# Performance work log

Hardware: AMD Instinct MI355X
Metric: run time of the kernel (lower is better)

## Reference

```python
import jax, jax.numpy as jnp
import numpy as np

GRID_SIZE = 5
SPLINE_ORDER = 3
# Extended knot grid over [-1, 1]: grid_size + 2*spline_order + 1 = 12 knots
_H = 2.0 / GRID_SIZE
GRID = (jnp.arange(-SPLINE_ORDER, GRID_SIZE + SPLINE_ORDER + 1, dtype=jnp.float32) * _H - 1.0)


def b_splines(x):
    # x: [N, F] -> bases [N, F, GRID_SIZE + SPLINE_ORDER]
    g = GRID.astype(x.dtype)
    xe = x[..., None]
    bases = ((xe >= g[:-1]) & (xe < g[1:])).astype(x.dtype)
    for k in range(1, SPLINE_ORDER + 1):
        left = (xe - g[: -(k + 1)]) / (g[k:-1] - g[: -(k + 1)]) * bases[..., :-1]
        right = (g[k + 1:] - xe) / (g[k + 1:] - g[1:-k]) * bases[..., 1:]
        bases = left + right
    return bases


def kan_conv(x, base_w, spline_w, spline_scaler):
    # x: [B, Cin, H, W]; 3x3 conv, stride 1, pad 1 -> [B, Cout, H, W]
    B, C, H, W = x.shape
    patches = jax.lax.conv_general_dilated_patches(
        x, (3, 3), (1, 1), [(1, 1), (1, 1)])  # [B, C*9, H, W]
    feat = patches.transpose(0, 2, 3, 1).reshape(B * H * W, C * 9)
    base_out = jax.nn.silu(feat) @ base_w.T  # [N, Cout]
    bas = b_splines(feat)                    # [N, C*9, 8]
    sw = spline_w * spline_scaler[..., None] # standalone spline scale
    spline_out = jnp.einsum('nik,oik->no', bas, sw)
    out = (base_out + spline_out).reshape(B, H, W, -1).transpose(0, 3, 1, 2)
    return out


def upsample2x(x):
    return jnp.repeat(jnp.repeat(x, 2, axis=2), 2, axis=3)


def setup_inputs() -> dict:
    key = jax.random.key(0)
    ks = jax.random.split(key, 16)
    d = {}
    d['x'] = jax.random.normal(ks[0], (64, 100), dtype=jnp.float32)
    d['lin_w'] = jax.random.normal(ks[1], (2048, 100), dtype=jnp.float32) * 0.1
    d['lin_b'] = jax.random.normal(ks[2], (2048,), dtype=jnp.float32) * 0.01
    chans = [(512, 256), (256, 128), (128, 64), (64, 3)]
    i = 3
    for li, (cin, cout) in enumerate(chans, start=1):
        fin = cin * 9
        scale = 1.0 / np.sqrt(fin)
        d[f'bw{li}'] = jax.random.normal(ks[i], (cout, fin), dtype=jnp.float32) * scale; i += 1
        d[f'sw{li}'] = jax.random.normal(ks[i], (cout, fin, GRID_SIZE + SPLINE_ORDER), dtype=jnp.float32) * (0.1 * scale); i += 1
        d[f'ss{li}'] = jax.random.normal(ks[i], (cout, fin), dtype=jnp.float32) * scale + 1.0; i += 1
    return d


def reference(x, lin_w, lin_b, bw1, sw1, ss1, bw2, sw2, ss2, bw3, sw3, ss3, bw4, sw4, ss4):
    h = jax.nn.relu(x @ lin_w.T + lin_b)          # [B, 2048]
    h = h.reshape(-1, 512, 2, 2)                  # Unflatten
    h = upsample2x(h)                             # 4x4
    h = kan_conv(h, bw1, sw1, ss1)                # [B,256,4,4]
    h = upsample2x(h)                             # 8x8
    h = kan_conv(h, bw2, sw2, ss2)                # [B,128,8,8]
    h = upsample2x(h)                             # 16x16
    h = kan_conv(h, bw3, sw3, ss3)                # [B,64,16,16]
    h = upsample2x(h)                             # 32x32
    h = kan_conv(h, bw4, sw4, ss4)                # [B,3,32,32]
    return jnp.tanh(h)
```

## Files before the change

### kernel.cpp

```cpp
#include <hip/hip_runtime.h>
#include <cstdint>
#include <cmath>

#define BATCH 64

typedef __attribute__((ext_vector_type(8))) __bf16 bf16x8;
typedef __attribute__((ext_vector_type(16))) float f32x16;

__device__ __forceinline__ void expand9(float x, float* e) {
  float t = __expf(-x);
  e[0] = __fdividef(x, 1.f + t);
  float b[11];
#pragma unroll
  for (int j = 0; j < 11; ++j) {
    float gj  = 0.4f * (float)j - 2.2f;
    float gj1 = 0.4f * (float)(j + 1) - 2.2f;
    b[j] = (x >= gj && x < gj1) ? 1.f : 0.f;
  }
#pragma unroll
  for (int k = 1; k <= 3; ++k) {
    float inv = 1.f / (0.4f * (float)k);
#pragma unroll
    for (int j = 0; j < 11 - k; ++j) {
      float gj   = 0.4f * (float)j - 2.2f;
      float gjk1 = 0.4f * (float)(j + k + 1) - 2.2f;
      b[j] = ((x - gj) * b[j] + (gjk1 - x) * b[j + 1]) * inv;
    }
  }
#pragma unroll
  for (int v = 0; v < 8; ++v) e[v + 1] = b[v];
}

__device__ __forceinline__ unsigned short f2bf(float x) {
  uint32_t u = __float_as_uint(x);
  uint32_t r = u + 0x7fffu + ((u >> 16) & 1u);
  return (unsigned short)(r >> 16);
}

__device__ __forceinline__ void pack9(const float* e, uint32_t* d) {
  d[0] = (uint32_t)f2bf(e[0]) | ((uint32_t)f2bf(e[1]) << 16);
  d[1] = (uint32_t)f2bf(e[2]) | ((uint32_t)f2bf(e[3]) << 16);
  d[2] = (uint32_t)f2bf(e[4]) | ((uint32_t)f2bf(e[5]) << 16);
  d[3] = (uint32_t)f2bf(e[6]) | ((uint32_t)f2bf(e[7]) << 16);
  d[4] = (uint32_t)f2bf(e[8]);
}

template <int F, int N, int LOGN>
__device__ __forceinline__ void bpack_body(int bid, const float* __restrict__ bw,
                                           const float* __restrict__ sw,
                                           const float* __restrict__ ss,
                                           unsigned short* __restrict__ Bg) {
  int idx = bid * 256 + threadIdx.x;
  int fl = idx & 15;
  int n = (idx >> 4) & (N - 1);
  int kc = idx >> (4 + LOGN);
  int f = kc * 16 + fl;
  size_t src = (size_t)n * F + f;
  float bv = bw[src];
  float sc = ss[src];
  const float4* sp = reinterpret_cast<const float4*>(sw + src * 8);
  float4 s0 = sp[0], s1 = sp[1];
  size_t base = ((size_t)(kc * 9) * N + n) * 16 + fl;
  const size_t vs = (size_t)N * 16;
  Bg[base]          = f2bf(bv);
  Bg[base + vs]     = f2bf(s0.x * sc);
  Bg[base + 2 * vs] = f2bf(s0.y * sc);
  Bg[base + 3 * vs] = f2bf(s0.z * sc);
  Bg[base + 4 * vs] = f2bf(s0.w * sc);
  Bg[base + 5 * vs] = f2bf(s1.x * sc);
  Bg[base + 6 * vs] = f2bf(s1.y * sc);
  Bg[base + 7 * vs] = f2bf(s1.z * sc);
  Bg[base + 8 * vs] = f2bf(s1.w * sc);
}

__device__ __forceinline__ void wnl4_body(int bid, const float* __restrict__ bw,
                                          const float* __restrict__ sw,
                                          const float* __restrict__ ss,
                                          float* __restrict__ Wn) {
  int idx = bid * 256 + threadIdx.x;
  if (idx >= 27648) return;
  int u = idx % 27;
  int o = u % 3, v = u / 3;
  int rest = idx / 27;
  int nb = rest & 3;
  rest >>= 2;
  int pc = rest & 3;
  rest >>= 2;
  int c = rest;
  int PH = pc >> 1, PW = pc & 1;
  int a = nb >> 1, b2 = nb & 1;
  float s = 0.f;
#pragma unroll
  for (int kh = 0; kh < 3; ++kh) {
    if (((kh > PH) ? 1 : 0) != a) continue;
#pragma unroll
    for (int kw = 0; kw < 3; ++kw) {
      if (((kw > PW) ? 1 : 0) != b2) continue;
      int f = c * 9 + kh * 3 + kw;
      float wv = (v == 0)
                     ? bw[o * 576 + f]
                     : sw[((size_t)(o * 576 + f)) * 8 + (v - 1)] * ss[o * 576 + f];
      s += wv;
    }
  }
  Wn[idx] = s;
}

__device__ __forceinline__ void linear_body(int bid, const float* __restrict__ x,
                                            const float* __restrict__ w,
                                            const float* __restrict__ bias,
                                            float* __restrict__ h,
                                            uint32_t* __restrict__ E) {
  int idx = bid * 256 + threadIdx.x;
  int b = idx >> 11, o = idx & 2047;
  const float* xr = x + b * 100;
  const float* wr = w + o * 100;
  float acc = bias[o];
#pragma unroll 4
  for (int k = 0; k < 100; ++k) acc += xr[k] * wr[k];
  float hv = fmaxf(acc, 0.f);
  h[idx] = hv;
  float e[9];
  expand9(hv, e);
  uint32_t d[5];
  pack9(e, d);
  uint4* p = reinterpret_cast<uint4*>(E + (size_t)idx * 8);
  p[0] = make_uint4(d[0], d[1], d[2], d[3]);
  p[1] = make_uint4(d[4], 0u, 0u, 0u);
}

__global__ __launch_bounds__(256) void prep_all(
    const float* __restrict__ x, const float* __restrict__ lin_w,
    const float* __restrict__ lin_b, float* __restrict__ h,
    uint32_t* __restrict__ Eg,
    const float* __restrict__ bw1, const float* __restrict__ sw1,
    const float* __restrict__ ss1, unsigned short* __restrict__ Bg1,
    const float* __restrict__ bw2, const float* __restrict__ sw2,
    const float* __restrict__ ss2, unsigned short* __restrict__ Bg2,
    const float* __restrict__ bw3, const float* __restrict__ sw3,
    const float* __restrict__ ss3, unsigned short* __restrict__ Bg3,
    const float* __restrict__ bw4, const float* __restrict__ sw4,
    const float* __restrict__ ss4, float* __restrict__ wl4) {
  int bid = blockIdx.x;
  if (bid < 4608) { bpack_body<4608, 256, 8>(bid, bw1, sw1, ss1, Bg1); return; }
  bid -= 4608;
  if (bid < 1152) { bpack_body<2304, 128, 7>(bid, bw2, sw2, ss2, Bg2); return; }
  bid -= 1152;
  if (bid < 288) { bpack_body<1152, 64, 6>(bid, bw3, sw3, ss3, Bg3); return; }
  bid -= 288;
  if (bid < 108) { wnl4_body(bid, bw4, sw4, ss4, wl4); return; }
  bid -= 108;
  linear_body(bid, x, lin_w, lin_b, h, Eg);
}

__global__ __launch_bounds__(256) void linear_relu_only(
    const float* __restrict__ x, const float* __restrict__ w,
    const float* __restrict__ bias, float* __restrict__ h) {
  int idx = blockIdx.x * 256 + threadIdx.x;
  int b = idx >> 11, o = idx & 2047;
  const float* xr = x + b * 100;
  const float* wr = w + o * 100;
  float acc = bias[o];
#pragma unroll 4
  for (int k = 0; k < 100; ++k) acc += xr[k] * wr[k];
  h[idx] = fmaxf(acc, 0.f);
}

template <int CIN, int COUT, int HO, int WO, int SK>
__global__ __launch_bounds__(256, 4) void gemm_mfma(
    const uint32_t* __restrict__ E, const unsigned short* __restrict__ Bg,
    float* __restrict__ part) {
  constexpr int F = CIN * 9;
  constexpr int NKC = F / 16;
  constexpr int HI = HO / 2, WI = WO / 2;
  constexpr int M = BATCH * HO * WO;
  constexpr int CPB = NKC / SK;
  static_assert(NKC % SK == 0, "sk");

  __shared__ __align__(16) unsigned short lds[2 * 9216];

  const int t = threadIdx.x;
  const int mbase = blockIdx.x * 64;
  const int nb = blockIdx.y;
  const int kc0 = blockIdx.z * CPB;

  uint32_t ez[5];
  {
    float e0[9];
    expand9(0.f, e0);
    pack9(e0, ez);
  }

  const int lane = t & 63, wv_ = t >> 6;
  const int wm = wv_ >> 1, wn = wv_ & 1;
  const int frow = lane & 31, fkg = lane >> 5;
  const int aoff = ((wm * 32 + frow) * 16 + fkg * 8) * 2;
  const int boff = ((wn * 32 + frow) * 16 + fkg * 8) * 2;

  const int aml = t >> 2, flq = t & 3;
  const int am = mbase + aml;
  const int ab = am / (HO * WO), ahw = am % (HO * WO);
  const int ahh = ahw / WO, aww = ahw % WO;

  f32x16 acc;
#pragma unroll
  for (int i = 0; i < 16; ++i) acc[i] = 0.f;

  for (int ci = 0; ci < CPB; ++ci) {
    const int kc = kc0 + ci;
    __syncthreads();

    {
      uint32_t w0[5], w1[5], w2[5], w3[5];
#define LDTAP(IDX, DST)                                                       \
  {                                                                           \
    int f = kc * 16 + flq * 4 + IDX;                                          \
    int c = f / 9, r = f - 9 * c;                                             \
    int kh = r / 3, kw = r - kh * 3;                                          \
    int hp = ahh + kh - 1, wp = aww + kw - 1;                                 \
    if ((unsigned)hp < (unsigned)HO && (unsigned)wp < (unsigned)WO) {         \
      const uint32_t* ep =                                                    \
          E + (size_t)(((ab * CIN + c) * HI + (hp >> 1)) * WI + (wp >> 1)) *  \
                  8;                                                          \
      uint4 q0 = *reinterpret_cast<const uint4*>(ep);                         \
      DST[0] = q0.x; DST[1] = q0.y; DST[2] = q0.z; DST[3] = q0.w;             \
      DST[4] = ep[4];                                                         \
    } else {                                                                  \
      _Pragma("unroll") for (int v = 0; v < 5; ++v) DST[v] = ez[v];           \
    }                                                                         \
  }
      LDTAP(0, w0)
      LDTAP(1, w1)
      LDTAP(2, w2)
      LDTAP(3, w3)
#undef LDTAP
#define GETV(W, V) (((V)&1) ? ((W)[(V) >> 1] >> 16) : ((W)[(V) >> 1] & 0xffffu))
      char* lb = reinterpret_cast<char*>(lds);
#pragma unroll
      for (int v = 0; v < 9; ++v) {
        uint32_t t0 = GETV(w0, v), t1 = GETV(w1, v);
        uint32_t t2 = GETV(w2, v), t3 = GETV(w3, v);
        uint32_t hi01 = t0 | (t1 << 16);
        uint32_t hi23 = t2 | (t3 << 16);
        *reinterpret_cast<uint2*>(lb + v * 2048 + aml * 32 + flq * 8) =
            make_uint2(hi01, hi23);
      }
#undef GETV
    }

    {
      const unsigned short* bsrc = Bg + (size_t)kc * (9 * COUT * 16);
#define STAGEB(U)                                                             \
  {                                                                           \
    int u = (U);                                                              \
    int v = u >> 7, q = u & 127;                                              \
    int nl = q >> 1, half = q & 1;                                            \
    size_t srcE = (size_t)v * (COUT * 16) + (size_t)(nb * 64 + nl) * 16 +     \
                  half * 8;                                                   \
    int dst = 9216 + v * 1024 + nl * 16 + half * 8;                           \
    *reinterpret_cast<float4*>(&lds[dst]) =                                   \
        *reinterpret_cast<const float4*>(&bsrc[srcE]);                        \
  }
      STAGEB(t)
      STAGEB(256 + t)
      STAGEB(512 + t)
      STAGEB(768 + t)
      if (t < 128) STAGEB(1024 + t)
#undef STAGEB
    }
    __syncthreads();

#pragma unroll
    for (int v = 0; v < 9; ++v) {
      const char* lbc = reinterpret_cast<const char*>(lds);
      bf16x8 ah = *reinterpret_cast<const bf16x8*>(lbc + v * 2048 + aoff);
      bf16x8 bh =
          *reinterpret_cast<const bf16x8*>(lbc + 18432 + v * 2048 + boff);
      acc = __builtin_amdgcn_mfma_f32_32x32x16_bf16(ah, bh, acc, 0, 0, 0);
    }
  }

  float* p = part + (size_t)blockIdx.z * M * COUT;
  const int gn = nb * 64 + wn * 32 + frow;
#pragma unroll
  for (int r = 0; r < 16; ++r) {
    int mlocal = (r & 3) + 8 * (r >> 2) + 4 * fkg;
    int gm = mbase + wm * 32 + mlocal;
    p[(size_t)gm * COUT + gn] = acc[r];
  }
}

template <int COUT, int HO, int WO>
__global__ __launch_bounds__(256) void reduce_pe_pack(
    const float* __restrict__ part, uint32_t* __restrict__ E, int SK) {
  constexpr int M = BATCH * HO * WO;
  int idx = blockIdx.x * 256 + threadIdx.x;
  int ww = idx % WO;
  int tmp = idx / WO;
  int hh = tmp % HO;
  tmp /= HO;
  int o = tmp % COUT;
  int b = tmp / COUT;
  int m = (b * HO + hh) * WO + ww;
  float s = 0.f;
  for (int k = 0; k < SK; ++k) s += part[((size_t)k * M + m) * COUT + o];
  float e[9];
  expand9(s, e);
  uint32_t d[5];
  pack9(e, d);
  uint4* p = reinterpret_cast<uint4*>(E + (size_t)idx * 8);
  p[0] = make_uint4(d[0], d[1], d[2], d[3]);
  p[1] = make_uint4(d[4], 0u, 0u, 0u);
}

template <int COUT, int HO, int WO>
__global__ __launch_bounds__(256) void reduce_p(
    const float* __restrict__ part, float* __restrict__ act, int SK) {
  constexpr int M = BATCH * HO * WO;
  int idx = blockIdx.x * 256 + threadIdx.x;
  int ww = idx % WO;
  int tmp = idx / WO;
  int hh = tmp % HO;
  tmp /= HO;
  int o = tmp % COUT;
  int b = tmp / COUT;
  int m = (b * HO + hh) * WO + ww;
  float s = 0.f;
  for (int k = 0; k < SK; ++k) s += part[((size_t)k * M + m) * COUT + o];
  act[idx] = s;
}

template <int PH, int PW>
__device__ void l4v8_wave(const float* __restrict__ eLds,
                          const float* __restrict__ WnB,
                          const float* __restrict__ ez, int lane, int bb,
                          int cs, float* __restrict__ p4) {
  constexpr int PC = PH * 2 + PW;
  const int j = lane & 15;
  const int i0 = (lane >> 4) << 2;
#pragma unroll 1
  for (int q = 0; q < 4; ++q) {
    const int i = i0 + q;
    float acc[3] = {0.f, 0.f, 0.f};
#pragma unroll
    for (int a = 0; a < 2; ++a) {
      const int gi = i + PH - 1 + a;
      const bool vr = (unsigned)gi < 16u;
#pragma unroll
      for (int b2 = 0; b2 < 2; ++b2) {
        const int gj = j + PW - 1 + b2;
        const bool ok = vr && ((unsigned)gj < 16u);
        const int pp = ok ? (gi * 16 + gj) : 0;
        const int nbi = a * 2 + b2;
#pragma unroll
        for (int cl = 0; cl < 2; ++cl) {
          const float* ep = eLds + cl * 2304 + pp * 9;
          float en[9];
#pragma unroll
          for (int v = 0; v < 9; ++v) en[v] = ok ? ep[v] : ez[v];
          const float* wp = WnB + ((cl * 4 + PC) * 4 + nbi) * 27;
#pragma unroll
          for (int v = 0; v < 9; ++v) {
            acc[0] = fmaf(en[v], wp[v * 3 + 0], acc[0]);
            acc[1] = fmaf(en[v], wp[v * 3 + 1], acc[1]);
            acc[2] = fmaf(en[v], wp[v * 3 + 2], acc[2]);
          }
        }
      }
    }
    const int h = (i << 1) + PH, w = (j << 1) + PW;
#pragma unroll
    for (int o = 0; o < 3; ++o)
      p4[(size_t)cs * 196608 + ((bb * 3 + o) << 10) + (h << 5) + w] = acc[o];
  }
}

__global__ __launch_bounds__(256) void kan_l4_v8(
    const float* __restrict__ a3, const float* __restrict__ Wn,
    float* __restrict__ p4) {
  __shared__ float eLds[2 * 256 * 9];
  const int bid = blockIdx.x;
  const int bb = bid >> 5, cs = bid & 31;
  const int t = threadIdx.x;
  float ez[9];
  expand9(0.f, ez);
#pragma unroll
  for (int cl = 0; cl < 2; ++cl) {
    float x = a3[(size_t)(bb * 64 + cs * 2 + cl) * 256 + t];
    float ev[9];
    expand9(x, ev);
#pragma unroll
    for (int v = 0; v < 9; ++v) eLds[(cl * 256 + t) * 9 + v] = ev[v];
  }
  __syncthreads();
  const int wv_ = t >> 6, lane = t & 63;
  const float* WnB = Wn + (size_t)cs * 2 * (4 * 4 * 27);
  if (wv_ == 0)
    l4v8_wave<0, 0>(eLds, WnB, ez, lane, bb, cs, p4);
  else if (wv_ == 1)
    l4v8_wave<0, 1>(eLds, WnB, ez, lane, bb, cs, p4);
  else if (wv_ == 2)
    l4v8_wave<1, 0>(eLds, WnB, ez, lane, bb, cs, p4);
  else
    l4v8_wave<1, 1>(eLds, WnB, ez, lane, bb, cs, p4);
}

__global__ __launch_bounds__(256) void reduce_tanh_l4_32(
    const float* __restrict__ p4, float* __restrict__ out) {
  int i = blockIdx.x * 256 + threadIdx.x;
  float s = 0.f;
#pragma unroll
  for (int k = 0; k < 32; ++k) s += p4[(size_t)k * 196608 + i];
  out[i] = tanhf(s);
}

__global__ __launch_bounds__(256) void reduce_tanh_l4(
    const float* __restrict__ p4, float* __restrict__ out) {
  int i = blockIdx.x * 256 + threadIdx.x;
  float s = p4[i] + p4[i + 196608] + p4[i + 2 * 196608] + p4[i + 3 * 196608];
  out[i] = tanhf(s);
}

template <int CIN, int COUT, int HO, int WO, int BN, int SK>
__global__ __launch_bounds__(256) void kan_gemm(
    const float* __restrict__ in, const float* __restrict__ bw,
    const float* __restrict__ sw, const float* __restrict__ ss,
    float* __restrict__ outp) {
  constexpr int BM = 64, TM = 4, TN = 4, FC = 16;
  constexpr int F = CIN * 9;
  constexpr int HI = HO / 2, WI = WO / 2;
  constexpr int M = BATCH * HO * WO;
  constexpr int FPB = F / SK;

  __shared__ float Ae[FC * 9][BM];

  const int t = threadIdx.x;
  const int mbase = blockIdx.x * BM;
  const int obase = blockIdx.y * BN;
  const int f0 = blockIdx.z * FPB;

  const int cg = t & (BN / TN - 1);
  const int rg = t / (BN / TN);
  const int m0 = rg * TM;
  const int o0 = obase + cg * TN;

  float acc[TM][TN] = {};

  for (int fc = f0; fc < f0 + FPB; fc += FC) {
#pragma unroll
    for (int j = 0; j < BM * FC / 256; ++j) {
      int p = j * 256 + t;
      int ml = p & (BM - 1);
      int df = p >> 6;
      int f = fc + df;
      int c = f / 9;
      int r = f - c * 9;
      int kh = r / 3, kw = r - kh * 3;
      int m = mbase + ml;
      int bb = m / (HO * WO);
      int rem = m % (HO * WO);
      int hh = rem / WO, ww = rem % WO;
      int hp = hh + kh - 1, wp = ww + kw - 1;
      float val = 0.f;
      if (hp >= 0 && hp < HO && wp >= 0 && wp < WO)
        val = in[((bb * CIN + c) * HI + (hp >> 1)) * WI + (wp >> 1)];
      float e[9];
      expand9(val, e);
#pragma unroll
      for (int v = 0; v < 9; ++v) Ae[df * 9 + v][ml] = e[v];
    }
    __syncthreads();

#pragma unroll 2
    for (int df = 0; df < FC; ++df) {
      int f = fc + df;
      float wb[TN], wsv[TN][8];
#pragma unroll
      for (int tn = 0; tn < TN; ++tn) {
        int i = (o0 + tn) * F + f;
        wb[tn] = bw[i];
        float sc = ss[i];
        const float4* sp = reinterpret_cast<const float4*>(sw + (size_t)i * 8);
        float4 s0 = sp[0], s1 = sp[1];
        wsv[tn][0] = s0.x * sc; wsv[tn][1] = s0.y * sc;
        wsv[tn][2] = s0.z * sc; wsv[tn][3] = s0.w * sc;
        wsv[tn][4] = s1.x * sc; wsv[tn][5] = s1.y * sc;
        wsv[tn][6] = s1.z * sc; wsv[tn][7] = s1.w * sc;
      }
      float a[9][TM];
#pragma unroll
      for (int v = 0; v < 9; ++v) {
        float4 q = *reinterpret_cast<const float4*>(&Ae[df * 9 + v][m0]);
        a[v][0] = q.x; a[v][1] = q.y; a[v][2] = q.z; a[v][3] = q.w;
      }
#pragma unroll
      for (int tm = 0; tm < TM; ++tm)
#pragma unroll
        for (int tn = 0; tn < TN; ++tn) acc[tm][tn] += a[0][tm] * wb[tn];
#pragma unroll
      for (int v = 1; v < 9; ++v)
#pragma unroll
        for (int tm = 0; tm < TM; ++tm)
#pragma unroll
          for (int tn = 0; tn < TN; ++tn)
            acc[tm][tn] += a[v][tm] * wsv[tn][v - 1];
    }
    __syncthreads();
  }

  if constexpr (SK > 1) {
    float* p = outp + (size_t)blockIdx.z * M * COUT;
#pragma unroll
    for (int tm = 0; tm < TM; ++tm) {
      int m = mbase + m0 + tm;
#pragma unroll
      for (int tn = 0; tn < TN; ++tn)
        p[(size_t)m * COUT + (o0 + tn)] = acc[tm][tn];
    }
  } else {
#pragma unroll
    for (int tm = 0; tm < TM; ++tm) {
      int m = mbase + m0 + tm;
      int bb = m / (HO * WO);
      int rem = m % (HO * WO);
      int hh = rem / WO, ww = rem % WO;
#pragma unroll
      for (int tn = 0; tn < TN; ++tn) {
        int o = o0 + tn;
        outp[((bb * COUT + o) * HO + hh) * WO + ww] = acc[tm][tn];
      }
    }
  }
}

template <int COUT, int HO, int WO, int SK>
__global__ __launch_bounds__(256) void reduce_partials_old(
    const float* __restrict__ part, float* __restrict__ act) {
  constexpr int M = BATCH * HO * WO;
  int idx = blockIdx.x * 256 + threadIdx.x;
  if (idx >= M * COUT) return;
  float s = 0.f;
#pragma unroll
  for (int k = 0; k < SK; ++k) s += part[(size_t)k * M * COUT + idx];
  int m = idx / COUT, o = idx - (idx / COUT) * COUT;
  int bb = m / (HO * WO);
  int rem = m % (HO * WO);
  int hh = rem / WO, ww = rem % WO;
  act[((bb * COUT + o) * HO + hh) * WO + ww] = s;
}

__global__ __launch_bounds__(256) void kan_l4_split(
    const float* __restrict__ a3, const float* __restrict__ bw,
    const float* __restrict__ sw, const float* __restrict__ ss,
    float* __restrict__ p4) {
  int tid = blockIdx.x * 256 + threadIdx.x;
  int cs = tid >> 16, pix = tid & 65535;
  int b = pix >> 10, rem = pix & 1023, h = rem >> 5, w = rem & 31;
  float acc[3] = {0.f, 0.f, 0.f};
  for (int c = cs * 16; c < cs * 16 + 16; ++c) {
#pragma unroll
    for (int kh = 0; kh < 3; ++kh) {
#pragma unroll
      for (int kw = 0; kw < 3; ++kw) {
        int f = (c * 3 + kh) * 3 + kw;
        int hp = h + kh - 1, wp = w + kw - 1;
        float x = 0.f;
        if ((unsigned)hp < 32u && (unsigned)wp < 32u)
          x = a3[((b * 64 + c) * 16 + (hp >> 1)) * 16 + (wp >> 1)];
        float e[9];
        expand9(x, e);
#pragma unroll
        for (int o = 0; o < 3; ++o) {
          int i = o * 576 + f;
          float d = e[1] * sw[i * 8 + 0];
#pragma unroll
          for (int v = 1; v < 8; ++v) d += e[v + 1] * sw[i * 8 + v];
          acc[o] += e[0] * bw[i] + d * ss[i];
        }
      }
    }
  }
#pragma unroll
  for (int o = 0; o < 3; ++o)
    p4[cs * 196608 + ((b * 3 + o) << 10) + (h << 5) + w] = acc[o];
}

extern "C" void kernel_launch(void* const* d_in, const int* in_sizes, int n_in,
                              void* d_out, int out_size, void* d_ws,
                              size_t ws_size, hipStream_t stream) {
  const float* x     = (const float*)d_in[0];
  const float* lin_w = (const float*)d_in[1];
  const float* lin_b = (const float*)d_in[2];
  const float* bw1 = (const float*)d_in[3];
  const float* sw1 = (const float*)d_in[4];
  const float* ss1 = (const float*)d_in[5];
  const float* bw2 = (const float*)d_in[6];
  const float* sw2 = (const float*)d_in[7];
  const float* ss2 = (const float*)d_in[8];
  const float* bw3 = (const float*)d_in[9];
  const float* sw3 = (const float*)d_in[10];
  const float* ss3 = (const float*)d_in[11];
  const float* bw4 = (const float*)d_in[12];
  const float* sw4 = (const float*)d_in[13];
  const float* ss4 = (const float*)d_in[14];

  float* wsf = (float*)d_ws;
  float* h    = wsf;
  float* a3   = wsf + 131072;
  unsigned short* Bg1 = (unsigned short*)(wsf + 1179648);
  unsigned short* Bg2 = (unsigned short*)(wsf + 6488064);
  unsigned short* Bg3 = (unsigned short*)(wsf + 7815168);
  float* wl4  = wsf + 8146944;
  float* part = wsf + 8174592;
  uint32_t* Eg = (uint32_t*)(wsf + 12368896);
  float* p4   = wsf + 8174592;

  const size_t mainNeed = 16563200ull;

  if (ws_size / 4 >= mainNeed) {
    prep_all<<<6668, 256, 0, stream>>>(
        x, lin_w, lin_b, h, Eg,
        bw1, sw1, ss1, Bg1,
        bw2, sw2, ss2, Bg2,
        bw3, sw3, ss3, Bg3,
        bw4, sw4, ss4, wl4);

    gemm_mfma<512, 256, 4, 4, 16>
        <<<dim3(16, 4, 16), 256, 0, stream>>>(Eg, Bg1, part);
    reduce_pe_pack<256, 4, 4><<<1024, 256, 0, stream>>>(part, Eg, 16);

    gemm_mfma<256, 128, 8, 8, 8>
        <<<dim3(64, 2, 8), 256, 0, stream>>>(Eg, Bg2, part);
    reduce_pe_pack<128, 8, 8><<<2048, 256, 0, stream>>>(part, Eg, 8);

    gemm_mfma<128, 64, 16, 16, 4>
        <<<dim3(256, 1, 4), 256, 0, stream>>>(Eg, Bg3, part);
    reduce_p<64, 16, 16><<<4096, 256, 0, stream>>>(part, a3, 4);

    kan_l4_v8<<<2048, 256, 0, stream>>>(a3, wl4, p4);
    reduce_tanh_l4_32<<<768, 256, 0, stream>>>(p4, (float*)d_out);
  } else {
    float* hF  = wsf;
    float* a1F = hF + 131072;
    float* a2F = a1F + 262144;
    float* a3F = a2F + 524288;
    float* partOld = a3F + 1048576;
    linear_relu_only<<<512, 256, 0, stream>>>(x, lin_w, lin_b, hF);
    kan_gemm<512, 256, 4, 4, 64, 8>
        <<<dim3(16, 4, 8), 256, 0, stream>>>(hF, bw1, sw1, ss1, partOld);
    reduce_partials_old<256, 4, 4, 8><<<1024, 256, 0, stream>>>(partOld, a1F);
    kan_gemm<256, 128, 8, 8, 64, 2>
        <<<dim3(64, 2, 2), 256, 0, stream>>>(a1F, bw2, sw2, ss2, partOld);
    reduce_partials_old<128, 8, 8, 2><<<2048, 256, 0, stream>>>(partOld, a2F);
    kan_gemm<128, 64, 16, 16, 64, 1>
        <<<dim3(256, 1, 1), 256, 0, stream>>>(a2F, bw3, sw3, ss3, a3F);
    kan_l4_split<<<1024, 256, 0, stream>>>(a3F, bw4, sw4, ss4, partOld);
    reduce_tanh_l4<<<768, 256, 0, stream>>>(partOld, (float*)d_out);
  }
}
```

Baseline: 287.8 us.

## Coalesce split-K reduction reads and split layer-4 conv blocks in half

The split-K reduction kernels now walk the partial buffers in their native row-major order, so loads are contiguous, and scatter the result into the channel-major layout. Before, the loads were strided and the stores contiguous. The layer-4 kernel is split so each block computes half of the rows per wave, doubling the grid from 2048 to 4096 blocks for more parallelism. The cost is that each block recomputes the shared spline expansion, and the reduction kernels now do scattered writes.

```diff
diff --git a/kernel.cpp b/kernel.cpp
--- a/kernel.cpp
+++ b/kernel.cpp
@@ -295,20 +295,18 @@
     const float* __restrict__ part, uint32_t* __restrict__ E, int SK) {
   constexpr int M = BATCH * HO * WO;
   int idx = blockIdx.x * 256 + threadIdx.x;
-  int ww = idx % WO;
-  int tmp = idx / WO;
-  int hh = tmp % HO;
-  tmp /= HO;
-  int o = tmp % COUT;
-  int b = tmp / COUT;
-  int m = (b * HO + hh) * WO + ww;
   float s = 0.f;
-  for (int k = 0; k < SK; ++k) s += part[((size_t)k * M + m) * COUT + o];
+  for (int k = 0; k < SK; ++k) s += part[(size_t)k * M * COUT + idx];
+  int o = idx & (COUT - 1);
+  int m = idx / COUT;
+  int b = m / (HO * WO);
+  int hw = m % (HO * WO);
+  int idx2 = ((b * COUT + o) * (HO * WO)) + hw;
   float e[9];
   expand9(s, e);
   uint32_t d[5];
   pack9(e, d);
-  uint4* p = reinterpret_cast<uint4*>(E + (size_t)idx * 8);
+  uint4* p = reinterpret_cast<uint4*>(E + (size_t)idx2 * 8);
   p[0] = make_uint4(d[0], d[1], d[2], d[3]);
   p[1] = make_uint4(d[4], 0u, 0u, 0u);
 }
@@ -318,28 +316,25 @@
     const float* __restrict__ part, float* __restrict__ act, int SK) {
   constexpr int M = BATCH * HO * WO;
   int idx = blockIdx.x * 256 + threadIdx.x;
-  int ww = idx % WO;
-  int tmp = idx / WO;
-  int hh = tmp % HO;
-  tmp /= HO;
-  int o = tmp % COUT;
-  int b = tmp / COUT;
-  int m = (b * HO + hh) * WO + ww;
   float s = 0.f;
-  for (int k = 0; k < SK; ++k) s += part[((size_t)k * M + m) * COUT + o];
-  act[idx] = s;
+  for (int k = 0; k < SK; ++k) s += part[(size_t)k * M * COUT + idx];
+  int o = idx & (COUT - 1);
+  int m = idx / COUT;
+  int b = m / (HO * WO);
+  int hw = m % (HO * WO);
+  act[((b * COUT + o) * (HO * WO)) + hw] = s;
 }
 
 template <int PH, int PW>
-__device__ void l4v8_wave(const float* __restrict__ eLds,
+__device__ void l4v9_wave(const float* __restrict__ eLds,
                           const float* __restrict__ WnB,
                           const float* __restrict__ ez, int lane, int bb,
-                          int cs, float* __restrict__ p4) {
+                          int cs, int qh, float* __restrict__ p4) {
   constexpr int PC = PH * 2 + PW;
   const int j = lane & 15;
   const int i0 = (lane >> 4) << 2;
 #pragma unroll 1
-  for (int q = 0; q < 4; ++q) {
+  for (int q = 2 * qh; q < 2 * qh + 2; ++q) {
     const int i = i0 + q;
     float acc[3] = {0.f, 0.f, 0.f};
 #pragma unroll
@@ -375,12 +370,12 @@
   }
 }
 
-__global__ __launch_bounds__(256) void kan_l4_v8(
+__global__ __launch_bounds__(256) void kan_l4_v9(
     const float* __restrict__ a3, const float* __restrict__ Wn,
     float* __restrict__ p4) {
   __shared__ float eLds[2 * 256 * 9];
   const int bid = blockIdx.x;
-  const int bb = bid >> 5, cs = bid & 31;
+  const int qh = bid & 1, cs = (bid >> 1) & 31, bb = bid >> 6;
   const int t = threadIdx.x;
   float ez[9];
   expand9(0.f, ez);
@@ -396,13 +391,13 @@
   const int wv_ = t >> 6, lane = t & 63;
   const float* WnB = Wn + (size_t)cs * 2 * (4 * 4 * 27);
   if (wv_ == 0)
-    l4v8_wave<0, 0>(eLds, WnB, ez, lane, bb, cs, p4);
+    l4v9_wave<0, 0>(eLds, WnB, ez, lane, bb, cs, qh, p4);
   else if (wv_ == 1)
-    l4v8_wave<0, 1>(eLds, WnB, ez, lane, bb, cs, p4);
+    l4v9_wave<0, 1>(eLds, WnB, ez, lane, bb, cs, qh, p4);
   else if (wv_ == 2)
-    l4v8_wave<1, 0>(eLds, WnB, ez, lane, bb, cs, p4);
+    l4v9_wave<1, 0>(eLds, WnB, ez, lane, bb, cs, qh, p4);
   else
-    l4v8_wave<1, 1>(eLds, WnB, ez, lane, bb, cs, p4);
+    l4v9_wave<1, 1>(eLds, WnB, ez, lane, bb, cs, qh, p4);
 }
 
 __global__ __launch_bounds__(256) void reduce_tanh_l4_32(
@@ -637,7 +632,7 @@
         <<<dim3(256, 1, 4), 256, 0, stream>>>(Eg, Bg3, part);
     reduce_p<64, 16, 16><<<4096, 256, 0, stream>>>(part, a3, 4);
 
-    kan_l4_v8<<<2048, 256, 0, stream>>>(a3, wl4, p4);
+    kan_l4_v9<<<4096, 256, 0, stream>>>(a3, wl4, p4);
     reduce_tanh_l4_32<<<768, 256, 0, stream>>>(p4, (float*)d_out);
   } else {
     float* hF  = wsf;
```

After: 258.7 us. -10.1%, faster.
